# Kernel tuning notes

Measured on AMD Instinct MI355X. Metric: run time of the kernel, lower is better.

The kernel has to match this reference:

```python
import jax, jax.numpy as jnp
import numpy as np

BIG = 1.0e6  # cost for empty groups
EPS = 1e-6

COST_ACTIVITY = 1.0
COST_GROUP = 1.0
COST_SIZE = 1.0


def setup_inputs() -> dict:
    key = jax.random.key(0)
    k1, k2, k3, k4 = jax.random.split(key, 4)
    bs, Q, C = 256, 512, 128   # batch, num_queries, num_activity_classes
    P, G = 256, 128            # num_persons, num_target_groups
    return {
        "pred_activity_logits": jax.random.normal(k1, (bs, Q, C), dtype=jnp.float32),
        "attention_logits": jax.random.normal(k2, (bs, P, Q), dtype=jnp.float32),
        "tgt_activity_ids": jax.random.randint(k3, (bs, G), 0, C),
        "tgt_group_ids": jax.random.randint(k4, (bs, P), 0, G),
    }


def reference(pred_activity_logits, attention_logits, tgt_activity_ids, tgt_group_ids):
    bs, Q, C = pred_activity_logits.shape
    P = attention_logits.shape[1]
    G = tgt_activity_ids.shape[1]

    # out_attw_b.T -> [Q, P]; log_softmax over dim 0 (queries)
    attw = jnp.transpose(attention_logits, (0, 2, 1))          # [bs, Q, P]
    logP = jax.nn.log_softmax(attw, axis=1)                    # softmax over queries
    P_qn = jnp.exp(logP)
    P_clamped = jnp.clip(P_qn, EPS, 1.0 - EPS)
    lognegP = jnp.log1p(-P_clamped)                            # [bs, Q, P]

    # one-hot grouping target: M[b, p, g] = 1 iff person p in group g
    M = jax.nn.one_hot(tgt_group_ids, G, dtype=logP.dtype)     # [bs, P, G]
    m = M.sum(axis=1)                                          # [bs, G] members per group
    nm = P - m                                                 # nonmembers per group

    # grouping cost: -mean member logP - mean nonmember log(1-P)
    mem_sum = jnp.einsum('bqp,bpg->bqg', logP, M)
    non_sum = jnp.einsum('bqp,bpg->bqg', lognegP, 1.0 - M)
    safe_m = jnp.maximum(m, 1.0)[:, None, :]
    safe_nm = jnp.maximum(nm, 1.0)[:, None, :]
    grouping_cost = -mem_sum / safe_m - non_sum / safe_nm      # [bs, Q, G]

    # size cost: |sum_p P_qn - m| / n_person
    pred_size = P_qn.sum(axis=2)                               # [bs, Q]
    size_cost = jnp.abs(pred_size[:, :, None] - m[:, None, :]) / max(float(P), 1.0)

    empty = (m == 0)[:, None, :]                               # [bs, 1, G]
    grouping_cost = jnp.where(empty, BIG, grouping_cost)
    size_cost = jnp.where(empty, BIG, size_cost)

    # activity cost: cross-entropy of query logits vs each group's activity class
    logq = jax.nn.log_softmax(pred_activity_logits, axis=-1)   # [bs, Q, C]
    idx = jnp.broadcast_to(tgt_activity_ids[:, None, :], (bs, Q, G))
    activity_cost = -jnp.take_along_axis(logq, idx, axis=2)    # [bs, Q, G]

    cost = (COST_GROUP * grouping_cost
            + COST_ACTIVITY * activity_cost
            + COST_SIZE * size_cost)
    return cost
```

## Files before the change

### kernel.cpp

```cpp
#include <hip/hip_runtime.h>

#define BS 256
#define NQ 512
#define NC 128
#define NP 256
#define NG 128
#define TQ 32
#define BIGC 1.0e6f
#define EPSC 1e-6f

__global__ __launch_bounds__(256) void lse_kernel(const float* __restrict__ att,
                                                  float* __restrict__ lse) {
    const int t   = threadIdx.x;
    const int row = blockIdx.x * 16 + (t >> 4);
    const int sub = t & 15;
    const float4* a4 = (const float4*)(att + (size_t)row * NQ);
    float4 v[8];
#pragma unroll
    for (int i = 0; i < 8; ++i) v[i] = a4[sub + 16 * i];
    float mx = -1e30f;
#pragma unroll
    for (int i = 0; i < 8; ++i)
        mx = fmaxf(mx, fmaxf(fmaxf(v[i].x, v[i].y), fmaxf(v[i].z, v[i].w)));
#pragma unroll
    for (int off = 1; off < 16; off <<= 1) mx = fmaxf(mx, __shfl_xor(mx, off, 64));
    float s = 0.f;
#pragma unroll
    for (int i = 0; i < 8; ++i)
        s += __expf(v[i].x - mx) + __expf(v[i].y - mx) + __expf(v[i].z - mx) + __expf(v[i].w - mx);
#pragma unroll
    for (int off = 1; off < 16; off <<= 1) s += __shfl_xor(s, off, 64);
    if (sub == 0) lse[row] = mx + __logf(s);
}

__global__ __launch_bounds__(256) void cost_kernel(
    const float* __restrict__ predAct,
    const float* __restrict__ att,
    const int*   __restrict__ actIds,
    const int*   __restrict__ grpIds,
    const float* __restrict__ lseAtt,
    float*       __restrict__ out)
{
    __shared__ float xS[NP * TQ];
    __shared__ float lseS[NP];
    __shared__ float lseAct[TQ];
    __shared__ float sumL1p[TQ];
    __shared__ float predSz[TQ];
    __shared__ int   gidS[NP];
    __shared__ int   memberS[NP];
    __shared__ int   aidS[NG];
    __shared__ int   cntS[NG];
    __shared__ int   startS[NG];
    __shared__ int   scanS[NG];

    const int b  = blockIdx.x >> 4;
    const int q0 = (blockIdx.x & 15) * TQ;
    const int t  = threadIdx.x;

    lseS[t] = lseAtt[b * NP + t];
    gidS[t] = grpIds[b * NP + t];
    if (t < NG) { aidS[t] = actIds[b * NG + t]; cntS[t] = 0; }
    if (t < TQ) { sumL1p[t] = 0.f; predSz[t] = 0.f; }
    __syncthreads();

    const int myPos = atomicAdd(&cntS[gidS[t]], 1);

    const int pr  = t >> 3;
    const int qo4 = (t & 7) * 4;
    float pl[4] = {0.f, 0.f, 0.f, 0.f};
    float ps[4] = {0.f, 0.f, 0.f, 0.f};
#pragma unroll
    for (int iter = 0; iter < 8; ++iter) {
        const int p = iter * 32 + pr;
        float4 v = *(const float4*)(att + ((size_t)(b * NP + p)) * NQ + q0 + qo4);
        const float l = lseS[p];
        float xv[4] = {v.x - l, v.y - l, v.z - l, v.w - l};
        *(float4*)(xS + p * TQ + qo4) = *(float4*)xv;
#pragma unroll
        for (int j = 0; j < 4; ++j) {
            float e = __expf(xv[j]);
            ps[j] += e;
            float c = fminf(fmaxf(e, EPSC), 1.f - EPSC);
            pl[j] += __logf(1.f - c);
        }
    }
#pragma unroll
    for (int j = 0; j < 4; ++j) {
#pragma unroll
        for (int off = 8; off < 64; off <<= 1) {
            pl[j] += __shfl_xor(pl[j], off, 64);
            ps[j] += __shfl_xor(ps[j], off, 64);
        }
    }
    if ((t & 63) < 8) {
#pragma unroll
        for (int j = 0; j < 4; ++j) {
            atomicAdd(&sumL1p[qo4 + j], pl[j]);
            atomicAdd(&predSz[qo4 + j], ps[j]);
        }
    }

    const int wv = t >> 6, ln = t & 63;
    for (int r = wv; r < TQ; r += 4) {
        const float* rowp = predAct + ((size_t)(b * NQ + q0 + r)) * NC;
        const float v0 = rowp[ln], v1 = rowp[ln + 64];
        float mx = fmaxf(v0, v1);
#pragma unroll
        for (int off = 1; off < 64; off <<= 1) mx = fmaxf(mx, __shfl_xor(mx, off, 64));
        float s = __expf(v0 - mx) + __expf(v1 - mx);
#pragma unroll
        for (int off = 1; off < 64; off <<= 1) s += __shfl_xor(s, off, 64);
        if (ln == 0) lseAct[r] = mx + __logf(s);
    }
    __syncthreads();

    if (t < NG) scanS[t] = cntS[t];
    __syncthreads();
    for (int off = 1; off < NG; off <<= 1) {
        int v = 0;
        if (t < NG && t >= off) v = scanS[t - off];
        __syncthreads();
        if (t < NG) scanS[t] += v;
        __syncthreads();
    }
    if (t < NG) startS[t] = scanS[t] - cntS[t];
    __syncthreads();
    memberS[startS[gidS[t]] + myPos] = t;
    __syncthreads();

    const float* actBase = predAct + ((size_t)(b * NQ + q0)) * NC;
#pragma unroll
    for (int rep = 0; rep < 4; ++rep) {
        const int idx = rep * 256 + t;
        const int qo  = idx & 31;
        const int g4  = (idx >> 5) * 4;
        const float sl = sumL1p[qo], pz = predSz[qo], la = lseAct[qo];
        float res[4];
#pragma unroll
        for (int j = 0; j < 4; ++j) {
            const int g  = g4 + j;
            const int m  = cntS[g];
            const int st = startS[g];
            float ms = 0.f, ml = 0.f;
            for (int i = 0; i < m; ++i) {
                const int p = memberS[st + i];
                const float x = xS[p * TQ + qo];
                ms += x;
                const float e = __expf(x);
                const float c = fminf(fmaxf(e, EPSC), 1.f - EPSC);
                ml += __logf(1.f - c);
            }
            const float mf  = (float)m;
            const float nmf = (float)(NP - m);
            float grp = -ms / fmaxf(mf, 1.f) - (sl - ml) / fmaxf(nmf, 1.f);
            float szc = fabsf(pz - mf) * (1.f / (float)NP);
            if (m == 0) { grp = BIGC; szc = BIGC; }
            const float av = actBase[(size_t)qo * NC + aidS[g]];
            res[j] = grp + (la - av) + szc;
        }
        *(float4*)(out + ((size_t)(b * NQ + q0 + qo)) * NG + g4) = *(float4*)res;
    }
}

extern "C" void kernel_launch(void* const* d_in, const int* in_sizes, int n_in,
                              void* d_out, int out_size, void* d_ws, size_t ws_size,
                              hipStream_t stream) {
    const float* predAct = (const float*)d_in[0];
    const float* att     = (const float*)d_in[1];
    const int*   actIds  = (const int*)d_in[2];
    const int*   grpIds  = (const int*)d_in[3];
    float*       out     = (float*)d_out;
    float*       lse     = (float*)d_ws;

    lse_kernel<<<BS * NP / 16, 256, 0, stream>>>(att, lse);
    cost_kernel<<<BS * (NQ / TQ), 256, 0, stream>>>(predAct, att, actIds, grpIds, lse, out);
}
```

Measured before the change: 341.1 us.

## Move per-query size/log1p sums into pre-kernel and sort xS by group rank

The LSE pre-kernel now also computes the per-query sums of P and log(1-P). Each 512-thread block handles 32 persons and writes partial sums to workspace. The cost kernel reduces those 8 partials instead of recomputing exp/log over all persons, and issues its attention loads early. It also replaces the multi-sync LDS scan with a wave shuffle scan and stores xS in group-sorted order, which removes the memberS indirection in the inner loop. This trades extra workspace traffic and shared atomics in the pre-kernel for less transcendental work and fewer barriers in the main kernel.

```diff
diff --git a/kernel.cpp b/kernel.cpp
--- a/kernel.cpp
+++ b/kernel.cpp
@@ -9,28 +9,69 @@
 #define BIGC 1.0e6f
 #define EPSC 1e-6f
 
-__global__ __launch_bounds__(256) void lse_kernel(const float* __restrict__ att,
-                                                  float* __restrict__ lse) {
+
+__global__ __launch_bounds__(512) void pre_kernel(const float* __restrict__ att,
+                                                  float* __restrict__ lse,
+                                                  float* __restrict__ part) {
+    __shared__ float szS[NQ];
+    __shared__ float slS[NQ];
     const int t   = threadIdx.x;
-    const int row = blockIdx.x * 16 + (t >> 4);
+    const int blk = blockIdx.x;
+    const int b   = blk >> 3;
+    const int p   = (blk & 7) * 32 + (t >> 4);
     const int sub = t & 15;
-    const float4* a4 = (const float4*)(att + (size_t)row * NQ);
+
+    szS[t] = 0.f;
+    slS[t] = 0.f;
+
+    const float4* a4 = (const float4*)(att + ((size_t)(b * NP + p)) * NQ);
     float4 v[8];
 #pragma unroll
     for (int i = 0; i < 8; ++i) v[i] = a4[sub + 16 * i];
+
     float mx = -1e30f;
 #pragma unroll
     for (int i = 0; i < 8; ++i)
         mx = fmaxf(mx, fmaxf(fmaxf(v[i].x, v[i].y), fmaxf(v[i].z, v[i].w)));
 #pragma unroll
     for (int off = 1; off < 16; off <<= 1) mx = fmaxf(mx, __shfl_xor(mx, off, 64));
+
     float s = 0.f;
 #pragma unroll
-    for (int i = 0; i < 8; ++i)
-        s += __expf(v[i].x - mx) + __expf(v[i].y - mx) + __expf(v[i].z - mx) + __expf(v[i].w - mx);
+    for (int i = 0; i < 8; ++i) {
+        v[i].x = __expf(v[i].x - mx); v[i].y = __expf(v[i].y - mx);
+        v[i].z = __expf(v[i].z - mx); v[i].w = __expf(v[i].w - mx);
+        s += v[i].x + v[i].y + v[i].z + v[i].w;
+    }
 #pragma unroll
     for (int off = 1; off < 16; off <<= 1) s += __shfl_xor(s, off, 64);
-    if (sub == 0) lse[row] = mx + __logf(s);
+    if (sub == 0) lse[b * NP + p] = mx + __logf(s);
+    const float inv = 1.f / s;
+
+    __syncthreads();
+
+#pragma unroll
+    for (int i = 0; i < 8; ++i) {
+        float Pv[4] = {v[i].x * inv, v[i].y * inv, v[i].z * inv, v[i].w * inv};
+#pragma unroll
+        for (int c = 0; c < 4; ++c) {
+            float P = Pv[c];
+            float Pc = fminf(fmaxf(P, EPSC), 1.f - EPSC);
+            float l = __logf(1.f - Pc);
+            P += __shfl_xor(P, 16, 64); P += __shfl_xor(P, 32, 64);
+            l += __shfl_xor(l, 16, 64); l += __shfl_xor(l, 32, 64);
+            if ((t & 63) < 16) {
+                const int q = 64 * i + 4 * sub + c;
+                atomicAdd(&szS[q], P);
+                atomicAdd(&slS[q], l);
+            }
+        }
+    }
+    __syncthreads();
+
+    float* basep = part + (size_t)blk * 2 * NQ;
+    basep[t]      = szS[t];
+    basep[NQ + t] = slS[t];
 }
 
 __global__ __launch_bounds__(256) void cost_kernel(
@@ -39,65 +80,69 @@
     const int*   __restrict__ actIds,
     const int*   __restrict__ grpIds,
     const float* __restrict__ lseAtt,
+    const float* __restrict__ part,
     float*       __restrict__ out)
 {
     __shared__ float xS[NP * TQ];
     __shared__ float lseS[NP];
     __shared__ float lseAct[TQ];
-    __shared__ float sumL1p[TQ];
-    __shared__ float predSz[TQ];
+    __shared__ float szG[TQ], slG[TQ];
     __shared__ int   gidS[NP];
-    __shared__ int   memberS[NP];
+    __shared__ int   rankS[NP];
     __shared__ int   aidS[NG];
     __shared__ int   cntS[NG];
     __shared__ int   startS[NG];
-    __shared__ int   scanS[NG];
 
     const int b  = blockIdx.x >> 4;
     const int q0 = (blockIdx.x & 15) * TQ;
     const int t  = threadIdx.x;
 
+    const int pr  = t >> 3;
+    const int qo4 = (t & 7) * 4;
+    float4 v[8];
+#pragma unroll
+    for (int iter = 0; iter < 8; ++iter)
+        v[iter] = *(const float4*)(att + ((size_t)(b * NP + iter * 32 + pr)) * NQ + q0 + qo4);
+
     lseS[t] = lseAtt[b * NP + t];
     gidS[t] = grpIds[b * NP + t];
     if (t < NG) { aidS[t] = actIds[b * NG + t]; cntS[t] = 0; }
-    if (t < TQ) { sumL1p[t] = 0.f; predSz[t] = 0.f; }
+    if (t < 2 * TQ) {
+        const int qo = t & 31, which = t >> 5;
+        const float* pb = part + ((size_t)(b * 8)) * 2 * NQ + (size_t)which * NQ + q0 + qo;
+        float s = 0.f;
+#pragma unroll
+        for (int k = 0; k < 8; ++k) s += pb[(size_t)k * 2 * NQ];
+        if (which == 0) szG[qo] = s; else slG[qo] = s;
+    }
     __syncthreads();
 
     const int myPos = atomicAdd(&cntS[gidS[t]], 1);
-
-    const int pr  = t >> 3;
-    const int qo4 = (t & 7) * 4;
-    float pl[4] = {0.f, 0.f, 0.f, 0.f};
-    float ps[4] = {0.f, 0.f, 0.f, 0.f};
+    __syncthreads();
+
+    if (t < 64) {
+        const int c0 = cntS[2 * t], c1 = cntS[2 * t + 1];
+        const int ps = c0 + c1;
+        int s = ps;
+#pragma unroll
+        for (int off = 1; off < 64; off <<= 1) {
+            const int w = __shfl_up(s, off, 64);
+            if (t >= off) s += w;
+        }
+        startS[2 * t]     = s - ps;
+        startS[2 * t + 1] = s - ps + c0;
+    }
+    __syncthreads();
+    rankS[t] = startS[gidS[t]] + myPos;
+    __syncthreads();
+
 #pragma unroll
     for (int iter = 0; iter < 8; ++iter) {
-        const int p = iter * 32 + pr;
-        float4 v = *(const float4*)(att + ((size_t)(b * NP + p)) * NQ + q0 + qo4);
+        const int p  = iter * 32 + pr;
         const float l = lseS[p];
-        float xv[4] = {v.x - l, v.y - l, v.z - l, v.w - l};
-        *(float4*)(xS + p * TQ + qo4) = *(float4*)xv;
-#pragma unroll
-        for (int j = 0; j < 4; ++j) {
-            float e = __expf(xv[j]);
-            ps[j] += e;
-            float c = fminf(fmaxf(e, EPSC), 1.f - EPSC);
-            pl[j] += __logf(1.f - c);
-        }
-    }
-#pragma unroll
-    for (int j = 0; j < 4; ++j) {
-#pragma unroll
-        for (int off = 8; off < 64; off <<= 1) {
-            pl[j] += __shfl_xor(pl[j], off, 64);
-            ps[j] += __shfl_xor(ps[j], off, 64);
-        }
-    }
-    if ((t & 63) < 8) {
-#pragma unroll
-        for (int j = 0; j < 4; ++j) {
-            atomicAdd(&sumL1p[qo4 + j], pl[j]);
-            atomicAdd(&predSz[qo4 + j], ps[j]);
-        }
+        const int rr = rankS[p];
+        float x[4] = {v[iter].x - l, v[iter].y - l, v[iter].z - l, v[iter].w - l};
+        *(float4*)(xS + rr * TQ + qo4) = *(float4*)x;
     }
 
     const int wv = t >> 6, ln = t & 63;
@@ -114,27 +159,13 @@
     }
     __syncthreads();
 
-    if (t < NG) scanS[t] = cntS[t];
-    __syncthreads();
-    for (int off = 1; off < NG; off <<= 1) {
-        int v = 0;
-        if (t < NG && t >= off) v = scanS[t - off];
-        __syncthreads();
-        if (t < NG) scanS[t] += v;
-        __syncthreads();
-    }
-    if (t < NG) startS[t] = scanS[t] - cntS[t];
-    __syncthreads();
-    memberS[startS[gidS[t]] + myPos] = t;
-    __syncthreads();
-
     const float* actBase = predAct + ((size_t)(b * NQ + q0)) * NC;
 #pragma unroll
     for (int rep = 0; rep < 4; ++rep) {
         const int idx = rep * 256 + t;
         const int qo  = idx & 31;
         const int g4  = (idx >> 5) * 4;
-        const float sl = sumL1p[qo], pz = predSz[qo], la = lseAct[qo];
+        const float sl = slG[qo], pz = szG[qo], la = lseAct[qo];
         float res[4];
 #pragma unroll
         for (int j = 0; j < 4; ++j) {
@@ -143,8 +174,7 @@
             const int st = startS[g];
             float ms = 0.f, ml = 0.f;
             for (int i = 0; i < m; ++i) {
-                const int p = memberS[st + i];
-                const float x = xS[p * TQ + qo];
+                const float x = xS[(st + i) * TQ + qo];
                 ms += x;
                 const float e = __expf(x);
                 const float c = fminf(fmaxf(e, EPSC), 1.f - EPSC);
@@ -171,7 +201,8 @@
     const int*   grpIds  = (const int*)d_in[3];
     float*       out     = (float*)d_out;
     float*       lse     = (float*)d_ws;
-
-    lse_kernel<<<BS * NP / 16, 256, 0, stream>>>(att, lse);
-    cost_kernel<<<BS * (NQ / TQ), 256, 0, stream>>>(predAct, att, actIds, grpIds, lse, out);
+    float*       part    = lse + (size_t)BS * NP;
+
+    pre_kernel<<<BS * 8, 512, 0, stream>>>(att, lse, part);
+    cost_kernel<<<BS * (NQ / TQ), 256, 0, stream>>>(predAct, att, actIds, grpIds, lse, part, out);
 }
```

Measured after the change: 402.0 us. 17.9% more time.
